# Optimization experiments

Hardware: AMD Instinct MI355X
Metric: run time of the kernel (lower is better)

## Reference

```python
import jax, jax.numpy as jnp
import numpy as np

N, E, D, DE, H, F, OUT = 50000, 800000, 256, 16, 4, 32, 32
SLOPE = 0.2


def setup_inputs() -> dict:
    key = jax.random.key(0)
    ks = jax.random.split(key, 16)
    inp = {
        "feat_src": jax.random.normal(ks[0], (N, D), jnp.float32),
        "feat_edge": jax.random.normal(ks[1], (E, DE), jnp.float32),
        "src_idx": jax.random.randint(ks[2], (E,), 0, N, jnp.int32),
        "dst_idx": jax.random.randint(ks[3], (E,), 0, N, jnp.int32),
        # parameters (xavier-ish scaling)
        "W_src": jax.random.normal(ks[4], (D, H * F), jnp.float32) * (2.0 / np.sqrt(D + H * F)),
        "W_attn_src": jax.random.normal(ks[5], (D, H), jnp.float32) * (2.0 / np.sqrt(D + H)),
        "W_attn_dst": jax.random.normal(ks[6], (D, H), jnp.float32) * (2.0 / np.sqrt(D + H)),
        "W_attn_edge": jax.random.normal(ks[7], (DE, H), jnp.float32) * (2.0 / np.sqrt(DE + H)),
        "scale": jnp.ones((1, H, F), jnp.float32),
        "offset": jnp.zeros((1, H, F), jnp.float32),
        "W_agg": jax.random.normal(ks[8], (H * F, H * F), jnp.float32) * (2.0 / np.sqrt(2 * H * F)),
        "b_agg": jnp.zeros((H * F,), jnp.float32),
        "W_dst": jax.random.normal(ks[9], (D, H * F), jnp.float32) * (2.0 / np.sqrt(D + H * F)),
        "b_dst": jnp.zeros((H * F,), jnp.float32),
        "W_apply": jax.random.normal(ks[10], (H * F, OUT), jnp.float32) * (2.0 / np.sqrt(H * F + OUT)),
        "b_apply": jnp.zeros((OUT,), jnp.float32),
    }
    return inp


def _leaky(x):
    return jnp.where(x >= 0, x, SLOPE * x)


def reference(feat_src, feat_edge, src_idx, dst_idx, W_src, W_attn_src, W_attn_dst,
              W_attn_edge, scale, offset, W_agg, b_agg, W_dst, b_dst, W_apply, b_apply):
    n = feat_src.shape[0]
    # node projections
    feat_src_fc = (feat_src @ W_src).reshape(n, H, F)          # [N,H,F]
    attn_src = (feat_src @ W_attn_src)[:, :, None]             # [N,H,1]
    attn_dst = (feat_src @ W_attn_dst)[:, :, None]             # feat_dst == feat_src (non-block)
    attn_edge = (feat_edge @ W_attn_edge)[:, :, None]          # [E,H,1]
    # per-edge attention logits: u_add_v + edge term, leaky_relu
    e = _leaky(attn_src[src_idx] + attn_dst[dst_idx] + attn_edge)  # [E,H,1]
    # segment softmax over incoming edges of each dst node ('single_softmax')
    e_max = jax.ops.segment_max(e, dst_idx, num_segments=n)        # [N,H,1]
    z = jnp.exp(e - e_max[dst_idx])
    z_sum = jax.ops.segment_sum(z, dst_idx, num_segments=n)
    a = z / z_sum[dst_idx]                                         # [E,H,1]
    # u_mul_e + sum aggregation
    msg = feat_src_fc[src_idx] * a                                 # [E,H,F]
    h = jax.ops.segment_sum(msg, dst_idx, num_segments=n)          # [N,H,F]
    # per-node per-head layernorm-like affine (agg_func, batch_norm=True)
    mean = jnp.mean(h, axis=-1, keepdims=True)
    var = jnp.mean((h - mean) ** 2, axis=-1, keepdims=True) + 1e-9
    h = (h - mean) * scale * jax.lax.rsqrt(var) + offset
    agg_msg = (h.reshape(n, H * F) @ W_agg + b_agg).reshape(n, H, F)
    # dst residual projection
    feat_dst_fc = (feat_src @ W_dst + b_dst).reshape(n, H, F)
    rst = _leaky(agg_msg + feat_dst_fc)
    rst = rst.reshape(n, H * F) @ W_apply + b_apply               # [N,OUT]
    return rst
```

## Files before the change

### kernel.cpp

```cpp
#include <hip/hip_runtime.h>
#include <hip/hip_fp16.h>

#define NN 50000
#define NE 800000
#define DD 256
#define DE_DIM 16
#define HH 4
#define FF 32
#define HF 128
#define OUTD 32
#define SLOPE 0.2f
#define NB_SCAN ((NN + 255) / 256)

#define BM 64
#define NCOL 272
#define APAD 264
#define BTPAD 40
#define TILE_S8 1088
#define NFB 64
#define FPAD 136

typedef short short8 __attribute__((ext_vector_type(8)));
typedef float f32x4 __attribute__((ext_vector_type(4)));
typedef unsigned short us4 __attribute__((ext_vector_type(4)));

__device__ __forceinline__ unsigned short bf16r(float x) {
  unsigned u = __float_as_uint(x);
  u += 0x7FFFu + ((u >> 16) & 1u);
  return (unsigned short)(u >> 16);
}
__device__ __forceinline__ float bfdec(unsigned short u) {
  return __uint_as_float(((unsigned)u) << 16);
}

__global__ __launch_bounds__(256) void bt_prep_kernel(
    const float* __restrict__ Wsrc, const float* __restrict__ Wdst,
    const float* __restrict__ Wasrc, const float* __restrict__ Wadst,
    unsigned short* __restrict__ Btt)
{
  int c = blockIdx.x;
  int k = threadIdx.x;
  float v = 0.f;
  if (c < 128)      v = Wsrc[(size_t)k * HF + c];
  else if (c < 256) v = Wdst[(size_t)k * HF + (c - 128)];
  else if (c < 260) v = Wasrc[(size_t)k * HH + (c - 256)];
  else if (c < 264) v = Wadst[(size_t)k * HH + (c - 260)];
  int kk = k >> 5, k5 = k & 31;
  Btt[(size_t)kk * (NCOL * 32) + c * 32 + k5] = bf16r(v);
}

__global__ __launch_bounds__(128) void wfin_prep_kernel(
    const float* __restrict__ W_agg, const float* __restrict__ W_apply,
    unsigned short* __restrict__ Wagg_t, unsigned short* __restrict__ Wapp_t)
{
  int c = blockIdx.x;
  int k = threadIdx.x;
  if (c < 128) Wagg_t[(size_t)c * HF + k] = bf16r(W_agg[(size_t)k * HF + c]);
  else         Wapp_t[(size_t)(c - 128) * HF + k] = bf16r(W_apply[(size_t)k * OUTD + (c - 128)]);
}

__global__ __launch_bounds__(512) void mfma_proj_kernel(
    const float* __restrict__ feat, const unsigned short* __restrict__ Btt,
    const float* __restrict__ bdst,
    unsigned short* __restrict__ fcs, unsigned short* __restrict__ fcd,
    float* __restrict__ asrc, float* __restrict__ adst)
{
  __shared__ unsigned short Albuf[BM * APAD];
  __shared__ unsigned short Btbuf[2][NCOL * BTPAD];
  const int tid  = threadIdx.x;
  const int wave = tid >> 6, lane = tid & 63;
  const int m0 = blockIdx.x * BM;

  for (int i = tid; i < BM * 64; i += 512) {
    int r = i >> 6, c4 = i & 63;
    int gr = m0 + r; if (gr >= NN) gr = NN - 1;
    float4 v = *(const float4*)(feat + (size_t)gr * DD + c4 * 4);
    us4 b; b.x = bf16r(v.x); b.y = bf16r(v.y); b.z = bf16r(v.z); b.w = bf16r(v.w);
    *(us4*)&Albuf[r * APAD + c4 * 4] = b;
  }

  const int ch0 = tid, ch1 = tid + 512, ch2 = tid + 1024;
  const short8* Bs8 = (const short8*)Btt;
  short8 st0, st1, st2;

  st0 = Bs8[ch0]; st1 = Bs8[ch1];
  if (ch2 < TILE_S8) st2 = Bs8[ch2];
  {
    int c, q;
    c = ch0 >> 2; q = ch0 & 3; *(short8*)&Btbuf[0][c * BTPAD + q * 8] = st0;
    c = ch1 >> 2; q = ch1 & 3; *(short8*)&Btbuf[0][c * BTPAD + q * 8] = st1;
    if (ch2 < TILE_S8) { c = ch2 >> 2; q = ch2 & 3; *(short8*)&Btbuf[0][c * BTPAD + q * 8] = st2; }
  }
  __syncthreads();

  const int r = wave >> 1, p = wave & 1;
  const int arow = r * 16 + (lane & 15);
  const int koff = (lane >> 4) * 8;
  const int cl = lane & 15;

  f32x4 acc[9];
#pragma unroll
  for (int t = 0; t < 9; ++t) acc[t] = (f32x4){0.f, 0.f, 0.f, 0.f};

  for (int kk = 0; kk < 8; ++kk) {
    const int cur = kk & 1;
    if (kk < 7) {
      const short8* src = Bs8 + (size_t)(kk + 1) * TILE_S8;
      st0 = src[ch0]; st1 = src[ch1];
      if (ch2 < TILE_S8) st2 = src[ch2];
    }
    short8 a = *(const short8*)&Albuf[arow * APAD + kk * 32 + koff];
#pragma unroll
    for (int t = 0; t < 9; ++t) {
      int c0 = p + 2 * t;
      if (c0 < 17) {
        short8 b = *(const short8*)&Btbuf[cur][(c0 * 16 + cl) * BTPAD + koff];
        acc[t] = __builtin_amdgcn_mfma_f32_16x16x32_bf16(a, b, acc[t], 0, 0, 0);
      }
    }
    if (kk < 7) {
      int c, q; const int nb = cur ^ 1;
      c = ch0 >> 2; q = ch0 & 3; *(short8*)&Btbuf[nb][c * BTPAD + q * 8] = st0;
      c = ch1 >> 2; q = ch1 & 3; *(short8*)&Btbuf[nb][c * BTPAD + q * 8] = st1;
      if (ch2 < TILE_S8) { c = ch2 >> 2; q = ch2 & 3; *(short8*)&Btbuf[nb][c * BTPAD + q * 8] = st2; }
    }
    __syncthreads();
  }

  const int rbase = m0 + r * 16 + (lane >> 4) * 4;
#pragma unroll
  for (int t = 0; t < 9; ++t) {
    int c0 = p + 2 * t;
    if (c0 >= 17) break;
    int gcol = c0 * 16 + cl;
#pragma unroll
    for (int j = 0; j < 4; ++j) {
      int grow = rbase + j;
      if (grow >= NN) continue;
      float v = acc[t][j];
      if (gcol < 128)      fcs[(size_t)grow * HF + gcol] = bf16r(v);
      else if (gcol < 256) fcd[(size_t)grow * HF + (gcol - 128)] = bf16r(v + bdst[gcol - 128]);
      else if (gcol < 260) asrc[(size_t)grow * HH + (gcol - 256)] = v;
      else if (gcol < 264) adst[(size_t)grow * HH + (gcol - 260)] = v;
    }
  }
}

__global__ __launch_bounds__(256) void edge_pre_kernel(
    const float* __restrict__ feat_edge, const float* __restrict__ Wae,
    const int* __restrict__ dst_idx, int* __restrict__ cnt,
    int* __restrict__ rank, uint2* __restrict__ aebuf)
{
  int e = blockIdx.x * 256 + threadIdx.x;
  if (e >= NE) return;

  float ae[HH] = {0.f, 0.f, 0.f, 0.f};
  const float4* fe4 = (const float4*)(feat_edge + (size_t)e * DE_DIM);
#pragma unroll
  for (int q = 0; q < 4; ++q) {
    float4 x = fe4[q];
    const float xs[4] = {x.x, x.y, x.z, x.w};
#pragma unroll
    for (int kk = 0; kk < 4; ++kk) {
      int k = q * 4 + kk;
#pragma unroll
      for (int h = 0; h < HH; ++h) ae[h] += xs[kk] * Wae[k * HH + h];
    }
  }
  __half2 a01 = __floats2half2_rn(ae[0], ae[1]);
  __half2 a23 = __floats2half2_rn(ae[2], ae[3]);
  uint2 u; u.x = *(unsigned*)&a01; u.y = *(unsigned*)&a23;
  aebuf[e] = u;
  rank[e] = atomicAdd(&cnt[dst_idx[e]], 1);
}

__global__ __launch_bounds__(256) void scan_block_kernel(
    const int* __restrict__ cnt, int* __restrict__ offs, int* __restrict__ bsum)
{
  __shared__ int tmp[256];
  int t = threadIdx.x;
  int i = blockIdx.x * 256 + t;
  int v = (i < NN) ? cnt[i] : 0;
  tmp[t] = v;
  __syncthreads();
  for (int ofs = 1; ofs < 256; ofs <<= 1) {
    int add = (t >= ofs) ? tmp[t - ofs] : 0;
    __syncthreads();
    tmp[t] += add;
    __syncthreads();
  }
  if (i < NN) offs[i] = tmp[t] - v;
  if (t == 255) bsum[blockIdx.x] = tmp[255];
}

__global__ __launch_bounds__(256) void scan_bsum_kernel(
    const int* __restrict__ bsum, int* __restrict__ boff)
{
  __shared__ int tmp[256];
  int t = threadIdx.x;
  int v = (t < NB_SCAN) ? bsum[t] : 0;
  tmp[t] = v;
  __syncthreads();
  for (int ofs = 1; ofs < 256; ofs <<= 1) {
    int add = (t >= ofs) ? tmp[t - ofs] : 0;
    __syncthreads();
    tmp[t] += add;
    __syncthreads();
  }
  if (t < NB_SCAN) boff[t] = tmp[t] - v;
}

__global__ __launch_bounds__(256) void scan_final_kernel(
    int* __restrict__ offs, const int* __restrict__ boff)
{
  int i = blockIdx.x * 256 + threadIdx.x;
  if (i < NN) offs[i] += boff[blockIdx.x];
  if (i == 0) offs[NN] = NE;
}

__global__ __launch_bounds__(256) void scatter_rec_kernel(
    const int* __restrict__ src_idx, const int* __restrict__ dst_idx,
    const float* __restrict__ asrc, const float* __restrict__ adst,
    const int* __restrict__ offs, const int* __restrict__ rank,
    const uint2* __restrict__ aebuf, int4* __restrict__ sorted)
{
  int e = blockIdx.x * 256 + threadIdx.x;
  if (e >= NE) return;
  int s = src_idx[e], d = dst_idx[e];

  uint2 u = aebuf[e];
  __half2 a01 = *(__half2*)&u.x;
  __half2 a23 = *(__half2*)&u.y;
  float ae[4];
  ae[0] = __low2float(a01); ae[1] = __high2float(a01);
  ae[2] = __low2float(a23); ae[3] = __high2float(a23);

  float as[4], ad[4];
  *(float4*)as = *(const float4*)(asrc + (size_t)s * 4);
  *(float4*)ad = *(const float4*)(adst + (size_t)d * 4);

  float ev[4];
#pragma unroll
  for (int h = 0; h < HH; ++h) {
    float v = as[h] + ad[h] + ae[h];
    ev[h] = v >= 0.f ? v : SLOPE * v;
  }
  __half2 p01 = __floats2half2_rn(ev[0], ev[1]);
  __half2 p23 = __floats2half2_rn(ev[2], ev[3]);
  int4 rec;
  rec.x = s;
  rec.y = *(int*)&p01;
  rec.z = *(int*)&p23;
  rec.w = 0;
  sorted[offs[d] + rank[e]] = rec;
}

__global__ __launch_bounds__(64) void agg_fused_kernel(
    const int* __restrict__ offs, const int4* __restrict__ sorted,
    const unsigned short* __restrict__ fcs, unsigned short* __restrict__ h_out)
{
  const int d = blockIdx.x;
  const int t = threadIdx.x;
  const int fpair = t << 1;
  const int h = t >> 4;
  const int beg = offs[d], end = offs[d + 1];
  const bool hiw = (h & 1);
  const bool hi2 = (h & 2);

  float ssum = 0.f, accx = 0.f, accy = 0.f;

  auto dec = [&](int4 r) -> float {
    int ew = hi2 ? r.z : r.y;
    __half2 hp = *(__half2*)&ew;
    return hiw ? __high2float(hp) : __low2float(hp);
  };

  int p = beg;
  for (; p + 4 <= end; p += 4) {
    int4 r0 = sorted[p + 0];
    int4 r1 = sorted[p + 1];
    int4 r2 = sorted[p + 2];
    int4 r3 = sorted[p + 3];
    unsigned f0 = *(const unsigned*)&fcs[(size_t)r0.x * HF + fpair];
    unsigned f1 = *(const unsigned*)&fcs[(size_t)r1.x * HF + fpair];
    unsigned f2 = *(const unsigned*)&fcs[(size_t)r2.x * HF + fpair];
    unsigned f3 = *(const unsigned*)&fcs[(size_t)r3.x * HF + fpair];
    float z0 = __expf(dec(r0));
    float z1 = __expf(dec(r1));
    float z2 = __expf(dec(r2));
    float z3 = __expf(dec(r3));
    ssum += (z0 + z1) + (z2 + z3);
    accx += bfdec((unsigned short)(f0 & 0xffff)) * z0
          + bfdec((unsigned short)(f1 & 0xffff)) * z1
          + bfdec((unsigned short)(f2 & 0xffff)) * z2
          + bfdec((unsigned short)(f3 & 0xffff)) * z3;
    accy += bfdec((unsigned short)(f0 >> 16)) * z0
          + bfdec((unsigned short)(f1 >> 16)) * z1
          + bfdec((unsigned short)(f2 >> 16)) * z2
          + bfdec((unsigned short)(f3 >> 16)) * z3;
  }
  for (; p < end; ++p) {
    int4 r0 = sorted[p];
    unsigned f0 = *(const unsigned*)&fcs[(size_t)r0.x * HF + fpair];
    float z = __expf(dec(r0));
    ssum += z;
    accx += bfdec((unsigned short)(f0 & 0xffff)) * z;
    accy += bfdec((unsigned short)(f0 >> 16)) * z;
  }
  float inv = (end > beg) ? 1.f / ssum : 0.f;
  ushort2 st;
  st.x = bf16r(accx * inv);
  st.y = bf16r(accy * inv);
  *(ushort2*)&h_out[(size_t)d * HF + fpair] = st;
}

__global__ __launch_bounds__(256) void node_final_mfma_kernel(
    const unsigned short* __restrict__ h_in, const float* __restrict__ scale,
    const float* __restrict__ offset,
    const unsigned short* __restrict__ Wagg_t, const float* __restrict__ b_agg,
    const unsigned short* __restrict__ fcd,
    const unsigned short* __restrict__ Wapp_t, const float* __restrict__ b_apply,
    float* __restrict__ out)
{
  __shared__ unsigned short Abuf[NFB * FPAD];
  __shared__ unsigned short Bagg[HF * FPAD];
  const int tid = threadIdx.x;
  const int wave = tid >> 6, lane = tid & 63;
  const int n0 = blockIdx.x * NFB;

  for (int i = tid; i < HF * 16; i += 256) {
    int c = i >> 4, q = i & 15;
    *(short8*)&Bagg[c * FPAD + q * 8] = *(const short8*)(Wagg_t + (size_t)c * HF + q * 8);
  }

  {
    const int r = tid >> 2, h = tid & 3;
    int node = n0 + r; if (node >= NN) node = NN - 1;
    const short8* hp = (const short8*)(h_in + (size_t)node * HF + h * 32);
    short8 v0 = hp[0], v1 = hp[1], v2 = hp[2], v3 = hp[3];

    float x[32];
#pragma unroll
    for (int j = 0; j < 8; ++j) {
      x[j]      = bfdec((unsigned short)v0[j]);
      x[8 + j]  = bfdec((unsigned short)v1[j]);
      x[16 + j] = bfdec((unsigned short)v2[j]);
      x[24 + j] = bfdec((unsigned short)v3[j]);
    }
    float sum = 0.f;
#pragma unroll
    for (int j = 0; j < 32; ++j) sum += x[j];
    float mean = sum * (1.f / 32.f);
    float sq = 0.f;
#pragma unroll
    for (int j = 0; j < 32; ++j) { float dv = x[j] - mean; sq += dv * dv; }
    float rsig = rsqrtf(sq * (1.f / 32.f) + 1e-9f);

#pragma unroll
    for (int c = 0; c < 4; ++c) {
      float4 s0 = *(const float4*)&scale[h * 32 + c * 8];
      float4 s1 = *(const float4*)&scale[h * 32 + c * 8 + 4];
      float4 o0 = *(const float4*)&offset[h * 32 + c * 8];
      float4 o1 = *(const float4*)&offset[h * 32 + c * 8 + 4];
      const float ss[8] = {s0.x, s0.y, s0.z, s0.w, s1.x, s1.y, s1.z, s1.w};
      const float oo[8] = {o0.x, o0.y, o0.z, o0.w, o1.x, o1.y, o1.z, o1.w};
      short8 w;
#pragma unroll
      for (int j = 0; j < 8; ++j)
        w[j] = (short)bf16r((x[c * 8 + j] - mean) * ss[j] * rsig + oo[j]);
      *(short8*)&Abuf[r * FPAD + h * 32 + c * 8] = w;
    }
  }
  __syncthreads();

  const int arow = wave * 16 + (lane & 15);
  const int koff = (lane >> 4) * 8;
  const int rbase = wave * 16 + (lane >> 4) * 4;
  const int cl = lane & 15;

  f32x4 acc1[8];
#pragma unroll
  for (int c0 = 0; c0 < 8; ++c0) acc1[c0] = (f32x4){0.f, 0.f, 0.f, 0.f};
#pragma unroll
  for (int ks = 0; ks < 4; ++ks) {
    short8 a = *(const short8*)&Abuf[arow * FPAD + ks * 32 + koff];
#pragma unroll
    for (int c0 = 0; c0 < 8; ++c0) {
      short8 b = *(const short8*)&Bagg[(c0 * 16 + cl) * FPAD + ks * 32 + koff];
      acc1[c0] = __builtin_amdgcn_mfma_f32_16x16x32_bf16(a, b, acc1[c0], 0, 0, 0);
    }
  }

#pragma unroll
  for (int c0 = 0; c0 < 8; ++c0) {
    int gcol = c0 * 16 + cl;
    float bg = b_agg[gcol];
#pragma unroll
    for (int j = 0; j < 4; ++j) {
      int row = rbase + j;
      int grow = n0 + row;
      float fd = (grow < NN) ? bfdec(fcd[(size_t)grow * HF + gcol]) : 0.f;
      float r = acc1[c0][j] + bg + fd;
      Abuf[row * FPAD + gcol] = bf16r(r >= 0.f ? r : SLOPE * r);
    }
  }

  f32x4 acc2[2];
#pragma unroll
  for (int c0 = 0; c0 < 2; ++c0) acc2[c0] = (f32x4){0.f, 0.f, 0.f, 0.f};
#pragma unroll
  for (int ks = 0; ks < 4; ++ks) {
    short8 a = *(const short8*)&Abuf[arow * FPAD + ks * 32 + koff];
#pragma unroll
    for (int c0 = 0; c0 < 2; ++c0) {
      short8 b = *(const short8*)(Wapp_t + (size_t)(c0 * 16 + cl) * HF + ks * 32 + koff);
      acc2[c0] = __builtin_amdgcn_mfma_f32_16x16x32_bf16(a, b, acc2[c0], 0, 0, 0);
    }
  }
#pragma unroll
  for (int c0 = 0; c0 < 2; ++c0) {
    int gcol = c0 * 16 + cl;
    float ba = b_apply[gcol];
#pragma unroll
    for (int j = 0; j < 4; ++j) {
      int grow = n0 + rbase + j;
      if (grow < NN) out[(size_t)grow * OUTD + gcol] = acc2[c0][j] + ba;
    }
  }
}

extern "C" void kernel_launch(void* const* d_in, const int* in_sizes, int n_in,
                              void* d_out, int out_size, void* d_ws, size_t ws_size,
                              hipStream_t stream)
{
  const float* feat_src    = (const float*)d_in[0];
  const float* feat_edge   = (const float*)d_in[1];
  const int*   src_idx     = (const int*)d_in[2];
  const int*   dst_idx     = (const int*)d_in[3];
  const float* W_src       = (const float*)d_in[4];
  const float* W_attn_src  = (const float*)d_in[5];
  const float* W_attn_dst  = (const float*)d_in[6];
  const float* W_attn_edge = (const float*)d_in[7];
  const float* scale       = (const float*)d_in[8];
  const float* offset      = (const float*)d_in[9];
  const float* W_agg       = (const float*)d_in[10];
  const float* b_agg       = (const float*)d_in[11];
  const float* W_dst       = (const float*)d_in[12];
  const float* b_dst       = (const float*)d_in[13];
  const float* W_apply     = (const float*)d_in[14];
  const float* b_apply     = (const float*)d_in[15];
  float* out = (float*)d_out;

  char* ws = (char*)d_ws;
  size_t off = 0;
  auto take = [&](size_t bytes) {
    size_t o = off;
    off = (off + bytes + 255) & ~(size_t)255;
    return o;
  };
  size_t fcs_off    = take((size_t)NN * HF * 2);
  size_t fcd_off    = take((size_t)NN * HF * 2);
  size_t asrc_off   = take((size_t)NN * 4 * 4);
  size_t adst_off   = take((size_t)NN * 4 * 4);
  size_t bt_off     = take((size_t)NCOL * DD * 2);
  size_t wagg_off   = take((size_t)HF * HF * 2);
  size_t wapp_off   = take((size_t)OUTD * HF * 2);
  size_t cnt_off    = take((size_t)NN * 4);
  size_t offs_off   = take((size_t)(NN + 1) * 4);
  size_t bsum_off   = take((size_t)NB_SCAN * 4);
  size_t boff_off   = take((size_t)NB_SCAN * 4);
  size_t rank_off   = take((size_t)NE * 4);
  size_t ae_off     = take((size_t)NE * 8);
  size_t sorted_off = take((size_t)NE * 16);
  size_t hout_off   = take((size_t)NN * HF * 2);
  if (ws_size < off) return;

  unsigned short* fcs    = (unsigned short*)(ws + fcs_off);
  unsigned short* fcd    = (unsigned short*)(ws + fcd_off);
  float*          asrc   = (float*)(ws + asrc_off);
  float*          adst   = (float*)(ws + adst_off);
  unsigned short* Btt    = (unsigned short*)(ws + bt_off);
  unsigned short* Wagg_t = (unsigned short*)(ws + wagg_off);
  unsigned short* Wapp_t = (unsigned short*)(ws + wapp_off);
  int*            cnt    = (int*)(ws + cnt_off);
  int*            offs   = (int*)(ws + offs_off);
  int*            bsum   = (int*)(ws + bsum_off);
  int*            boff   = (int*)(ws + boff_off);
  int*            rank   = (int*)(ws + rank_off);
  uint2*          aebuf  = (uint2*)(ws + ae_off);
  int4*           sorted = (int4*)(ws + sorted_off);
  unsigned short* h_out  = (unsigned short*)(ws + hout_off);

  hipMemsetAsync(ws + cnt_off, 0, (size_t)NN * 4, stream);

  bt_prep_kernel<<<NCOL, 256, 0, stream>>>(W_src, W_dst, W_attn_src, W_attn_dst, Btt);
  wfin_prep_kernel<<<160, 128, 0, stream>>>(W_agg, W_apply, Wagg_t, Wapp_t);

  edge_pre_kernel<<<(NE + 255) / 256, 256, 0, stream>>>(
      feat_edge, W_attn_edge, dst_idx, cnt, rank, aebuf);

  scan_block_kernel<<<NB_SCAN, 256, 0, stream>>>(cnt, offs, bsum);
  scan_bsum_kernel<<<1, 256, 0, stream>>>(bsum, boff);
  scan_final_kernel<<<NB_SCAN, 256, 0, stream>>>(offs, boff);

  mfma_proj_kernel<<<(NN + BM - 1) / BM, 512, 0, stream>>>(
      feat_src, Btt, b_dst, fcs, fcd, asrc, adst);

  scatter_rec_kernel<<<(NE + 255) / 256, 256, 0, stream>>>(
      src_idx, dst_idx, asrc, adst, offs, rank, aebuf, sorted);

  agg_fused_kernel<<<NN, 64, 0, stream>>>(offs, sorted, fcs, h_out);

  node_final_mfma_kernel<<<(NN + NFB - 1) / NFB, 256, 0, stream>>>(
      h_out, scale, offset, Wagg_t, b_agg, fcd, Wapp_t, b_apply, out);
}
```

Baseline: 171.2 us.

## Merge weight-prep kernels and co-schedule edge precompute with MFMA projection

Combines the two weight-transpose prep kernels into one launch. Also fuses the edge attention precompute (with the per-destination atomic counting) into the MFMA node-projection kernel by interleaving block roles: every third block does a projection tile and the other two process 512 edges each. This removes kernel launches and lets the memory-bound edge work overlap the compute-bound GEMM. In exchange, edge blocks carry the GEMM kernel's large shared-memory allocation and 512-thread launch bound, which may limit occupancy for them.

```diff
diff --git a/kernel.cpp b/kernel.cpp
--- a/kernel.cpp
+++ b/kernel.cpp
@@ -17,6 +17,8 @@
 #define APAD 264
 #define BTPAD 40
 #define TILE_S8 1088
+#define NMFMA 782
+#define NEDGE 1564
 #define NFB 64
 #define FPAD 136
 
@@ -33,43 +35,72 @@
   return __uint_as_float(((unsigned)u) << 16);
 }
 
-__global__ __launch_bounds__(256) void bt_prep_kernel(
+__global__ __launch_bounds__(256) void prep_kernel(
     const float* __restrict__ Wsrc, const float* __restrict__ Wdst,
     const float* __restrict__ Wasrc, const float* __restrict__ Wadst,
-    unsigned short* __restrict__ Btt)
-{
-  int c = blockIdx.x;
-  int k = threadIdx.x;
-  float v = 0.f;
-  if (c < 128)      v = Wsrc[(size_t)k * HF + c];
-  else if (c < 256) v = Wdst[(size_t)k * HF + (c - 128)];
-  else if (c < 260) v = Wasrc[(size_t)k * HH + (c - 256)];
-  else if (c < 264) v = Wadst[(size_t)k * HH + (c - 260)];
-  int kk = k >> 5, k5 = k & 31;
-  Btt[(size_t)kk * (NCOL * 32) + c * 32 + k5] = bf16r(v);
-}
-
-__global__ __launch_bounds__(128) void wfin_prep_kernel(
     const float* __restrict__ W_agg, const float* __restrict__ W_apply,
+    unsigned short* __restrict__ Btt,
     unsigned short* __restrict__ Wagg_t, unsigned short* __restrict__ Wapp_t)
 {
-  int c = blockIdx.x;
-  int k = threadIdx.x;
-  if (c < 128) Wagg_t[(size_t)c * HF + k] = bf16r(W_agg[(size_t)k * HF + c]);
-  else         Wapp_t[(size_t)(c - 128) * HF + k] = bf16r(W_apply[(size_t)k * OUTD + (c - 128)]);
-}
-
-__global__ __launch_bounds__(512) void mfma_proj_kernel(
+  int bid = blockIdx.x;
+  if (bid < NCOL) {
+    int c = bid, k = threadIdx.x;
+    float v = 0.f;
+    if (c < 128)      v = Wsrc[(size_t)k * HF + c];
+    else if (c < 256) v = Wdst[(size_t)k * HF + (c - 128)];
+    else if (c < 260) v = Wasrc[(size_t)k * HH + (c - 256)];
+    else if (c < 264) v = Wadst[(size_t)k * HH + (c - 260)];
+    int kk = k >> 5, k5 = k & 31;
+    Btt[(size_t)kk * (NCOL * 32) + c * 32 + k5] = bf16r(v);
+  } else {
+    int c = bid - NCOL, k = threadIdx.x;
+    if (k >= 128) return;
+    if (c < 128) Wagg_t[(size_t)c * HF + k] = bf16r(W_agg[(size_t)k * HF + c]);
+    else         Wapp_t[(size_t)(c - 128) * HF + k] = bf16r(W_apply[(size_t)k * OUTD + (c - 128)]);
+  }
+}
+
+__global__ __launch_bounds__(512) void fused_k1_kernel(
     const float* __restrict__ feat, const unsigned short* __restrict__ Btt,
     const float* __restrict__ bdst,
     unsigned short* __restrict__ fcs, unsigned short* __restrict__ fcd,
-    float* __restrict__ asrc, float* __restrict__ adst)
+    float* __restrict__ asrc, float* __restrict__ adst,
+    const float* __restrict__ feat_edge, const float* __restrict__ Wae,
+    const int* __restrict__ dst_idx, int* __restrict__ cnt,
+    int* __restrict__ rank, uint2* __restrict__ aebuf)
 {
   __shared__ unsigned short Albuf[BM * APAD];
   __shared__ unsigned short Btbuf[2][NCOL * BTPAD];
-  const int tid  = threadIdx.x;
+  const int bid = blockIdx.x;
+  const int tid = threadIdx.x;
+
+  if (bid % 3 != 0) {
+    int eid = bid - bid / 3 - 1;
+    int e = eid * 512 + tid;
+    if (e >= NE) return;
+    float ae[HH] = {0.f, 0.f, 0.f, 0.f};
+    const float4* fe4 = (const float4*)(feat_edge + (size_t)e * DE_DIM);
+#pragma unroll
+    for (int q = 0; q < 4; ++q) {
+      float4 x = fe4[q];
+      const float xs[4] = {x.x, x.y, x.z, x.w};
+#pragma unroll
+      for (int kk = 0; kk < 4; ++kk) {
+        int k = q * 4 + kk;
+#pragma unroll
+        for (int h = 0; h < HH; ++h) ae[h] += xs[kk] * Wae[k * HH + h];
+      }
+    }
+    __half2 a01 = __floats2half2_rn(ae[0], ae[1]);
+    __half2 a23 = __floats2half2_rn(ae[2], ae[3]);
+    uint2 u; u.x = *(unsigned*)&a01; u.y = *(unsigned*)&a23;
+    aebuf[e] = u;
+    rank[e] = atomicAdd(&cnt[dst_idx[e]], 1);
+    return;
+  }
+
   const int wave = tid >> 6, lane = tid & 63;
-  const int m0 = blockIdx.x * BM;
+  const int m0 = (bid / 3) * BM;
 
   for (int i = tid; i < BM * 64; i += 512) {
     int r = i >> 6, c4 = i & 63;
@@ -144,34 +175,6 @@
       else if (gcol < 264) adst[(size_t)grow * HH + (gcol - 260)] = v;
     }
   }
-}
-
-__global__ __launch_bounds__(256) void edge_pre_kernel(
-    const float* __restrict__ feat_edge, const float* __restrict__ Wae,
-    const int* __restrict__ dst_idx, int* __restrict__ cnt,
-    int* __restrict__ rank, uint2* __restrict__ aebuf)
-{
-  int e = blockIdx.x * 256 + threadIdx.x;
-  if (e >= NE) return;
-
-  float ae[HH] = {0.f, 0.f, 0.f, 0.f};
-  const float4* fe4 = (const float4*)(feat_edge + (size_t)e * DE_DIM);
-#pragma unroll
-  for (int q = 0; q < 4; ++q) {
-    float4 x = fe4[q];
-    const float xs[4] = {x.x, x.y, x.z, x.w};
-#pragma unroll
-    for (int kk = 0; kk < 4; ++kk) {
-      int k = q * 4 + kk;
-#pragma unroll
-      for (int h = 0; h < HH; ++h) ae[h] += xs[kk] * Wae[k * HH + h];
-    }
-  }
-  __half2 a01 = __floats2half2_rn(ae[0], ae[1]);
-  __half2 a23 = __floats2half2_rn(ae[2], ae[3]);
-  uint2 u; u.x = *(unsigned*)&a01; u.y = *(unsigned*)&a23;
-  aebuf[e] = u;
-  rank[e] = atomicAdd(&cnt[dst_idx[e]], 1);
 }
 
 __global__ __launch_bounds__(256) void scan_block_kernel(
@@ -493,19 +496,18 @@
 
   hipMemsetAsync(ws + cnt_off, 0, (size_t)NN * 4, stream);
 
-  bt_prep_kernel<<<NCOL, 256, 0, stream>>>(W_src, W_dst, W_attn_src, W_attn_dst, Btt);
-  wfin_prep_kernel<<<160, 128, 0, stream>>>(W_agg, W_apply, Wagg_t, Wapp_t);
-
-  edge_pre_kernel<<<(NE + 255) / 256, 256, 0, stream>>>(
+  prep_kernel<<<NCOL + 160, 256, 0, stream>>>(
+      W_src, W_dst, W_attn_src, W_attn_dst, W_agg, W_apply,
+      Btt, Wagg_t, Wapp_t);
+
+  fused_k1_kernel<<<NMFMA + NEDGE, 512, 0, stream>>>(
+      feat_src, Btt, b_dst, fcs, fcd, asrc, adst,
       feat_edge, W_attn_edge, dst_idx, cnt, rank, aebuf);
 
   scan_block_kernel<<<NB_SCAN, 256, 0, stream>>>(cnt, offs, bsum);
   scan_bsum_kernel<<<1, 256, 0, stream>>>(bsum, boff);
   scan_final_kernel<<<NB_SCAN, 256, 0, stream>>>(offs, boff);
 
-  mfma_proj_kernel<<<(NN + BM - 1) / BM, 512, 0, stream>>>(
-      feat_src, Btt, b_dst, fcs, fcd, asrc, adst);
-
   scatter_rec_kernel<<<(NE + 255) / 256, 256, 0, stream>>>(
       src_idx, dst_idx, asrc, adst, offs, rank, aebuf, sorted);
 
```

After: 149.8 us. 12.5% less time.
